# Optimization experiments

Measured on AMD Instinct MI355X. Metric: run time of the kernel, lower is better.

The kernel has to match this reference:

```python
import jax, jax.numpy as jnp
import numpy as np

NEG_SLOPE = 0.1

def mlp(x, w1, b1, w2, b2):
    # MLP(sizes): Linear -> LeakyReLU(0.1) -> Linear
    return jax.nn.leaky_relu(x @ w1 + b1, NEG_SLOPE) @ w2 + b2

def _seg_mean(vals, idx, n):
    s = jax.ops.segment_sum(vals, idx, num_segments=n)
    cnt = jax.ops.segment_sum(jnp.ones((vals.shape[0],), vals.dtype), idx, num_segments=n)
    return s / jnp.maximum(cnt, 1.0)[:, None]

def setup_inputs() -> dict:
    key = jax.random.key(0)
    ks = iter(jax.random.split(key, 40))
    N, F, H, E = 100000, 64, 128, 800000
    Ha = H // 2  # hidden_dim/2 = 64
    def lin(k, i, o):
        k1, k2 = jax.random.split(k)
        return (jax.random.normal(k1, (i, o), jnp.float32) * (1.0 / np.sqrt(i)),
                jax.random.normal(k2, (o,), jnp.float32) * 0.01)
    inp = {}
    inp['feat'] = jax.random.normal(next(ks), (N, F), jnp.float32)
    inp['pi_feat'] = jax.random.normal(next(ks), (N, 4), jnp.float32)
    inp['level'] = jax.random.uniform(next(ks), (N, 1), jnp.float32)
    inp['bit_position'] = jax.random.uniform(next(ks), (E, 1), jnp.float32)
    inp['is_po'] = jax.random.randint(next(ks), (N,), 0, 2, jnp.int32)
    inp['is_module'] = jax.random.randint(next(ks), (N,), 0, 2, jnp.int32)
    inp['src_m'] = jax.random.randint(next(ks), (E,), 0, N, jnp.int32)
    inp['dst_m'] = jax.random.randint(next(ks), (E,), 0, N, jnp.int32)
    inp['src_g'] = jax.random.randint(next(ks), (E,), 0, N, jnp.int32)
    inp['dst_g'] = jax.random.randint(next(ks), (E,), 0, N, jnp.int32)
    # mlp_pi: 4 -> H/2 -> H
    inp['pi_w1'], inp['pi_b1'] = lin(next(ks), 4, Ha)
    inp['pi_w2'], inp['pi_b2'] = lin(next(ks), Ha, H)
    # mlp_neigh_module: H + F + 1 -> H/2 -> H
    inp['nm_w1'], inp['nm_b1'] = lin(next(ks), H + F + 1, Ha)
    inp['nm_w2'], inp['nm_b2'] = lin(next(ks), Ha, H)
    # mlp_neigh_gate: H + F -> H/2 -> H
    inp['ng_w1'], inp['ng_b1'] = lin(next(ks), H + F, Ha)
    inp['ng_w2'], inp['ng_b2'] = lin(next(ks), Ha, H)
    # mlp_global: 1 -> H/2 -> H
    inp['g_w1'], inp['g_b1'] = lin(next(ks), 1, Ha)
    inp['g_w2'], inp['g_b2'] = lin(next(ks), Ha, H)
    # mlp_out: 2H -> H -> 1
    inp['o_w1'], inp['o_b1'] = lin(next(ks), 2 * H, H)
    inp['o_w2'], inp['o_b2'] = lin(next(ks), H, 1)
    return inp

def reference(feat, pi_feat, level, bit_position,
              pi_w1, pi_b1, pi_w2, pi_b2,
              nm_w1, nm_b1, nm_w2, nm_b2,
              ng_w1, ng_b1, ng_w2, ng_b2,
              g_w1, g_b1, g_w2, g_b2,
              o_w1, o_b1, o_w2, o_b2,
              is_po, is_module, src_m, dst_m, src_g, dst_g):
    N = feat.shape[0]
    # PI init embedding (mlp_pi)
    h0 = mlp(pi_feat, pi_w1, pi_b1, pi_w2, pi_b2)            # [N, H]
    # module-edge message passing: m = src h, pos = bit_position; mean reduce
    m = h0[src_m]                                            # [E, H] irregular gather
    neigh_m = _seg_mean(m, dst_m, N)                         # [N, H]
    pos_m = _seg_mean(bit_position, dst_m, N)                # [N, 1]
    # nodes_func_module, agg_choice==0: cat(neigh, pos, feat) -> mlp_neigh_module
    h_m = mlp(jnp.concatenate([neigh_m, pos_m, feat], axis=1), nm_w1, nm_b1, nm_w2, nm_b2)
    # gate-edge message passing
    neigh_g = _seg_mean(h0[src_g], dst_g, N)                 # [N, H]
    h_g = mlp(jnp.concatenate([neigh_g, feat], axis=1), ng_w1, ng_b1, ng_w2, ng_b2)
    # ReLU on non-PO nodes only
    keep = (is_po != 1)[:, None]
    h_m = jnp.where(keep, jax.nn.relu(h_m), h_m)
    h_g = jnp.where(keep, jax.nn.relu(h_g), h_g)
    # per-node-type update (hetero apply_nodes)
    h = jnp.where((is_module == 1)[:, None], h_m, h_g)       # [N, H]
    # global branch + readout
    hg = mlp(level, g_w1, g_b1, g_w2, g_b2)                  # [N, H]
    out = mlp(jnp.concatenate([h, hg], axis=1), o_w1, o_b1, o_w2, o_b2)  # [N, 1]
    return out
```

## Files before the change

### kernel.cpp

```cpp
#include <hip/hip_runtime.h>

typedef __bf16 bf16x8 __attribute__((ext_vector_type(8)));
typedef float f32x4 __attribute__((ext_vector_type(4)));
typedef unsigned short u16;
typedef unsigned int u32;
typedef unsigned long long u64;

__device__ __forceinline__ u16 f2b(float f) {
  return __builtin_bit_cast(u16, (__bf16)f);
}
__device__ __forceinline__ float b2f_lo(u32 pk) {
  return __builtin_bit_cast(float, pk << 16);
}
__device__ __forceinline__ float b2f_hi(u32 pk) {
  return __builtin_bit_cast(float, pk & 0xffff0000u);
}
__device__ __forceinline__ float leaky(float x) { return x > 0.f ? x : 0.1f * x; }
__device__ __forceinline__ f32x4 mfma16(bf16x8 a, bf16x8 b, f32x4 c) {
  return __builtin_amdgcn_mfma_f32_16x16x32_bf16(a, b, c, 0, 0, 0);
}

#define P64 72
#define P128 136
#define CAP 16
#define RSTRIDE 32

#define SBLK 256
#define PBLK 256

__global__ __launch_bounds__(256) void k_zero(int* rec, int* spillcnt, int N) {
  int n = blockIdx.x * 256 + threadIdx.x;
  if (n < N) {
    rec[(size_t)n * RSTRIDE] = 0;
    rec[(size_t)n * RSTRIDE + 1] = 0;
  }
  if (n == 0) *spillcnt = 0;
}

__global__ __launch_bounds__(256) void k_prep(
    const float* nm_w1, const float* ng_w1, const float* nm_w2, const float* ng_w2,
    const float* o_w1, const float* o_b1, const float* g_w2, const float* g_b2,
    const float* pi_w2, const float* pi_b2, const int* is_module,
    u16* wt_yc, float* bias_y, u16* wt_f1m, u16* wt_f1g, float* w_pos,
    u16* wt2m, u16* wt2g, u16* wt_oh, u16* gt, float* bp, u32* mbits, int N) {
  int i = blockIdx.x * 256 + threadIdx.x;
  if (i < 9216) {
    int ty = i / 4608, rem = i % 4608, n = rem / P64, k = rem % P64;
    float v = 0.f;
    if (k < 64) {
      const float* w1 = ty ? ng_w1 : nm_w1;
      for (int t = 0; t < 128; t++) v += pi_w2[k * 128 + t] * w1[t * 64 + n];
    }
    wt_yc[i] = f2b(v);
    return;
  }
  i -= 9216;
  if (i < 128) {
    int ty = i >> 6, n = i & 63;
    const float* w1 = ty ? ng_w1 : nm_w1;
    float v = 0.f;
    for (int t = 0; t < 128; t++) v += pi_b2[t] * w1[t * 64 + n];
    bias_y[i] = v;
    return;
  }
  i -= 128;
  if (i < 4608) {
    int n = i / P64, k = i % P64;
    wt_f1m[i] = f2b(k < 64 ? nm_w1[(129 + k) * 64 + n] : 0.f);
    return;
  }
  i -= 4608;
  if (i < 4608) {
    int n = i / P64, k = i % P64;
    wt_f1g[i] = f2b(k < 64 ? ng_w1[(128 + k) * 64 + n] : 0.f);
    return;
  }
  i -= 4608;
  if (i < 64) { w_pos[i] = nm_w1[128 * 64 + i]; return; }
  i -= 64;
  if (i < 9216) {
    int n = i / P64, k = i % P64;
    wt2m[i] = f2b(k < 64 ? nm_w2[k * 128 + n] : 0.f);
    return;
  }
  i -= 9216;
  if (i < 9216) {
    int n = i / P64, k = i % P64;
    wt2g[i] = f2b(k < 64 ? ng_w2[k * 128 + n] : 0.f);
    return;
  }
  i -= 9216;
  if (i < 17408) {
    int n = i / P128, k = i % P128;
    wt_oh[i] = f2b(k < 128 ? o_w1[k * 128 + n] : 0.f);
    return;
  }
  i -= 17408;
  if (i < 9216) {
    int n = i / P64, k = i % P64;
    float v = 0.f;
    if (k < 64)
      for (int t = 0; t < 128; t++) v += g_w2[k * 128 + t] * o_w1[(128 + t) * 128 + n];
    gt[i] = f2b(v);
    return;
  }
  i -= 9216;
  if (i < 128) {
    float s = o_b1[i];
    for (int t = 0; t < 128; t++) s += g_b2[t] * o_w1[(128 + t) * 128 + i];
    bp[i] = s;
    return;
  }
  i -= 128;
  {
    int n = i;
    int lane = threadIdx.x & 63;
    bool v = (n < N) && (is_module[n] == 1);
    u64 b = __ballot(v);
    if (lane == 0 && n < N) mbits[n >> 5] = (u32)b;
    if (lane == 32 && n < N) mbits[n >> 5] = (u32)(b >> 32);
  }
}

__global__ __launch_bounds__(512) void k_mid(
    const int* src_m, const int* dst_m, const int* src_g, const int* dst_g,
    const u32* mbits, const float* bitpos, int* rec, u64* spill, int* spillcnt,
    int E,
    const float* pf, const float* feat, const float* pi_w1, const float* pi_b1,
    const u16* wt_yc_g, const float* bias_y, const u16* wt_f1m_g, const u16* wt_f1g_g,
    const float* nm_b1, const float* ng_b1, u16* y0, u16* f1, int N) {
  __shared__ __align__(16) u16 wyc[2][64 * P64];
  __shared__ __align__(16) u16 wf[2][64 * P64];
  __shared__ __align__(16) u16 tbuf[8][16 * P64];

  if (blockIdx.x < SBLK) {
    int tid = blockIdx.x * 512 + threadIdx.x;
    const int STR = SBLK * 512;
    for (int v0 = tid; v0 < E; v0 += STR * 4) {
      int dd[8], ss[8];
      float bb[8];
      bool el[8];
#pragma unroll
      for (int k = 0; k < 4; k++) {
        int vt = v0 + k * STR;
        bool vv = vt < E;
#pragma unroll
        for (int j = 0; j < 2; j++) {
          int x = k * 2 + j;
          el[x] = false;
          dd[x] = 0; ss[x] = 0; bb[x] = 0.f;
          if (vv) {
            int e = vt * 2 + j;
            int d = (e < E) ? dst_m[e] : dst_g[e - E];
            dd[x] = d;
            bool bit = (mbits[d >> 5] >> (d & 31)) & 1;
            el[x] = (e < E) ? bit : !bit;
            if (el[x]) {
              if (e < E) { ss[x] = src_m[e]; bb[x] = bitpos[e]; }
              else ss[x] = src_g[e - E];
            }
          }
        }
      }
      int cc[8];
#pragma unroll
      for (int x = 0; x < 8; x++)
        if (el[x]) cc[x] = atomicAdd(&rec[(size_t)dd[x] * RSTRIDE], 1);
#pragma unroll
      for (int x = 0; x < 8; x++) {
        if (!el[x]) continue;
        int vt = v0 + (x >> 1) * STR;
        int e = vt * 2 + (x & 1);
        int d = dd[x], s = ss[x], c = cc[x];
        if (e < E) {
          if (c < CAP) {
            int bp12 = (int)(bb[x] * 4096.f);
            if (bp12 > 4095) bp12 = 4095;
            rec[(size_t)d * RSTRIDE + 2 + c] = (s << 12) | bp12;
          } else {
            int p = atomicAdd(spillcnt, 1);
            spill[p] = ((u64)(u32)d << 32) | (u32)s;
            atomicAdd((float*)&rec[(size_t)d * RSTRIDE + 1], bb[x]);
          }
        } else {
          if (c < CAP) {
            rec[(size_t)d * RSTRIDE + 2 + c] = s << 12;
          } else {
            int p = atomicAdd(spillcnt, 1);
            spill[p] = ((u64)(u32)d << 32) | (u32)s;
          }
        }
      }
    }
    return;
  }

  int pb = blockIdx.x - SBLK;
  for (int i = threadIdx.x; i < 2304; i += 512) {
    ((u32*)wyc[0])[i] = ((const u32*)wt_yc_g)[i];
    ((u32*)wyc[1])[i] = ((const u32*)wt_yc_g)[2304 + i];
    ((u32*)wf[0])[i] = ((const u32*)wt_f1m_g)[i];
    ((u32*)wf[1])[i] = ((const u32*)wt_f1g_g)[i];
  }

  int lane = threadIdx.x & 63, wv = threadIdx.x >> 6;
  int lid = lane & 15, q = lane >> 4;

  bf16x8 w1f[4];
#pragma unroll
  for (int nt = 0; nt < 4; nt++) {
    bf16x8 f;
#pragma unroll
    for (int j = 0; j < 8; j++) {
      int k = q * 8 + j;
      f[j] = (__bf16)((k < 4) ? pi_w1[k * 64 + nt * 16 + lid] : 0.f);
    }
    w1f[nt] = f;
  }
  __syncthreads();

  int nbat = (N + 15) >> 4;
  for (int b0 = pb * 8; b0 < nbat; b0 += PBLK * 8) {
    int b = b0 + wv;
    int batch = b < nbat ? b : nbat - 1;
    int id = batch * 16 + lid;
    if (id >= N) id = N - 1;

    bf16x8 a;
#pragma unroll
    for (int j = 0; j < 8; j++)
      a[j] = (__bf16)((q == 0 && j < 4) ? pf[(size_t)id * 4 + j] : 0.f);
    f32x4 z1[4];
#pragma unroll
    for (int nt = 0; nt < 4; nt++) {
      f32x4 c = {0.f, 0.f, 0.f, 0.f};
      z1[nt] = mfma16(a, w1f[nt], c);
    }
    __syncthreads();
#pragma unroll
    for (int nt = 0; nt < 4; nt++) {
      float bb = pi_b1[nt * 16 + lid];
#pragma unroll
      for (int r = 0; r < 4; r++)
        tbuf[wv][(q * 4 + r) * P64 + nt * 16 + lid] = f2b(leaky(z1[nt][r] + bb));
    }
    __syncthreads();
    bf16x8 a20 = *(const bf16x8*)&tbuf[wv][lid * P64 + q * 8];
    bf16x8 a21 = *(const bf16x8*)&tbuf[wv][lid * P64 + 32 + q * 8];

    int idr_[4];
#pragma unroll
    for (int r = 0; r < 4; r++) {
      int ii = batch * 16 + q * 4 + r;
      idr_[r] = ii < N ? ii : N - 1;
    }

#pragma unroll
    for (int ty = 0; ty < 2; ty++) {
#pragma unroll
      for (int nt = 0; nt < 4; nt++) {
        f32x4 c = {0.f, 0.f, 0.f, 0.f};
        c = mfma16(a20, *(const bf16x8*)&wyc[ty][(nt * 16 + lid) * P64 + q * 8], c);
        c = mfma16(a21, *(const bf16x8*)&wyc[ty][(nt * 16 + lid) * P64 + 32 + q * 8], c);
        float by = bias_y[ty * 64 + nt * 16 + lid];
#pragma unroll
        for (int r = 0; r < 4; r++)
          y0[(size_t)idr_[r] * 128 + ty * 64 + nt * 16 + lid] = f2b(c[r] + by);
      }
    }

    bf16x8 af[2];
#pragma unroll
    for (int kt = 0; kt < 2; kt++) {
      const float4* p = (const float4*)(feat + (size_t)id * 64 + kt * 32 + q * 8);
      float4 xa = p[0], xb = p[1];
      bf16x8 f;
      f[0] = (__bf16)xa.x; f[1] = (__bf16)xa.y; f[2] = (__bf16)xa.z; f[3] = (__bf16)xa.w;
      f[4] = (__bf16)xb.x; f[5] = (__bf16)xb.y; f[6] = (__bf16)xb.z; f[7] = (__bf16)xb.w;
      af[kt] = f;
    }
#pragma unroll
    for (int nt = 0; nt < 4; nt++) {
      f32x4 cm = {0.f, 0.f, 0.f, 0.f}, cg = {0.f, 0.f, 0.f, 0.f};
#pragma unroll
      for (int kt = 0; kt < 2; kt++) {
        cm = mfma16(af[kt], *(const bf16x8*)&wf[0][(nt * 16 + lid) * P64 + kt * 32 + q * 8], cm);
        cg = mfma16(af[kt], *(const bf16x8*)&wf[1][(nt * 16 + lid) * P64 + kt * 32 + q * 8], cg);
      }
      float bm = nm_b1[nt * 16 + lid], bg = ng_b1[nt * 16 + lid];
#pragma unroll
      for (int r = 0; r < 4; r++) {
        int idr = idr_[r];
        bool mod = (mbits[idr >> 5] >> (idr & 31)) & 1;
        f1[(size_t)idr * 64 + nt * 16 + lid] = f2b(mod ? cm[r] + bm : cg[r] + bg);
      }
    }
  }
}

__global__ __launch_bounds__(256) void k_gather(const u16* y0, const int* rec,
                                                const u64* spill, const int* spillcnt,
                                                const u32* mbits, const u16* f1,
                                                const float* w_pos, u16* z1a, int N) {
  int n = (blockIdx.x * 256 + threadIdx.x) >> 6;
  int lane = threadIdx.x & 63;
  if (n >= N) return;
  bool mod = (mbits[n >> 5] >> (n & 31)) & 1;
  int g = lane >> 4, l16 = lane & 15;
  int rv = (lane < 18) ? rec[(size_t)n * RSTRIDE + lane] : 0;
  int cnt = __shfl(rv, 0);
  float pspill = __builtin_bit_cast(float, __shfl(rv, 1));
  int inl = cnt < CAP ? cnt : CAP;
  float myb = 0.f;
  if (mod && lane >= 2 && lane < 18 && (lane - 2) < inl)
    myb = (float)(rv & 4095) * (1.f / 4096.f);
  const u32* yrow = (const u32*)y0;
  int halfo = mod ? 0 : 32;
  float a00 = 0.f, a01 = 0.f, a10 = 0.f, a11 = 0.f;
  for (int j = 0; j < inl; j += 4) {
    int e = j + g;
    if (e < inl) {
      int s = (int)(((u32)__shfl(rv, 2 + e)) >> 12);
      u64 pk = *(const u64*)(yrow + (size_t)s * 64 + halfo + 2 * l16);
      u32 p0 = (u32)pk, p1 = (u32)(pk >> 32);
      a00 += b2f_lo(p0); a01 += b2f_hi(p0);
      a10 += b2f_lo(p1); a11 += b2f_hi(p1);
    }
  }
  if (cnt > CAP) {
    int sc = *spillcnt;
    int idx = 0;
    for (int base = 0; base < sc; base += 64) {
      int i = base + lane;
      u64 ent = (i < sc) ? spill[i] : 0xffffffffffffffffull;
      bool m = ((int)(ent >> 32) == n);
      u64 bal = __ballot(m);
      int slo = (int)(ent & 0xffffffffu);
      while (bal) {
        int l = __ffsll((long long)bal) - 1;
        bal &= bal - 1;
        int s = __shfl(slo, l);
        if ((idx & 3) == g) {
          u64 pk = *(const u64*)(yrow + (size_t)s * 64 + halfo + 2 * l16);
          u32 p0 = (u32)pk, p1 = (u32)(pk >> 32);
          a00 += b2f_lo(p0); a01 += b2f_hi(p0);
          a10 += b2f_lo(p1); a11 += b2f_hi(p1);
        }
        idx++;
      }
    }
  }
  a00 += __shfl_xor(a00, 16); a00 += __shfl_xor(a00, 32);
  a01 += __shfl_xor(a01, 16); a01 += __shfl_xor(a01, 32);
  a10 += __shfl_xor(a10, 16); a10 += __shfl_xor(a10, 32);
  a11 += __shfl_xor(a11, 16); a11 += __shfl_xor(a11, 32);
#pragma unroll
  for (int off = 1; off < 64; off <<= 1) myb += __shfl_xor(myb, off);
  float psum = pspill + myb;
  float inv = 1.f / (float)(cnt > 1 ? cnt : 1);
  if (lane < 16) {
    u64 fp2 = *(const u64*)(((const u32*)f1) + (size_t)n * 32 + 2 * l16);
    u32 f0 = (u32)fp2, f1v = (u32)(fp2 >> 32);
    float z00 = a00 * inv + b2f_lo(f0);
    float z01 = a01 * inv + b2f_hi(f0);
    float z10 = a10 * inv + b2f_lo(f1v);
    float z11 = a11 * inv + b2f_hi(f1v);
    if (mod) {
      float pm = psum * inv;
      float4 wp = ((const float4*)w_pos)[l16];
      z00 += pm * wp.x; z01 += pm * wp.y;
      z10 += pm * wp.z; z11 += pm * wp.w;
    }
    u32 r0 = (u32)f2b(leaky(z00)) | ((u32)f2b(leaky(z01)) << 16);
    u32 r1 = (u32)f2b(leaky(z10)) | ((u32)f2b(leaky(z11)) << 16);
    *(u64*)(((u32*)z1a) + (size_t)n * 32 + 2 * l16) = ((u64)r1 << 32) | r0;
  }
}

__global__ __launch_bounds__(512) void k_tail(const u16* z1a, const u16* wt2m_g,
                                              const u16* wt2g_g, const float* nm_b2,
                                              const float* ng_b2, const u32* mbits,
                                              const int* is_po, const float* level,
                                              const float* g_w1, const float* g_b1,
                                              const u16* wt_oh_g, const u16* gt_g,
                                              const float* bp_g, const float* o_w2,
                                              const float* o_b2, float* out, int N) {
  __shared__ __align__(16) u16 w2[2][128 * P64];
  __shared__ __align__(16) u16 wt_oh[128 * P128];
  __shared__ __align__(16) u16 gt[128 * P64];
  __shared__ __align__(16) u16 tbuf[8][16 * P128];
  for (int i = threadIdx.x; i < 128 * P64 / 2; i += 512) {
    ((u32*)w2[0])[i] = ((const u32*)wt2m_g)[i];
    ((u32*)w2[1])[i] = ((const u32*)wt2g_g)[i];
    ((u32*)gt)[i] = ((const u32*)gt_g)[i];
  }
  for (int i = threadIdx.x; i < 128 * P128 / 2; i += 512)
    ((u32*)wt_oh)[i] = ((const u32*)wt_oh_g)[i];

  int lane = threadIdx.x & 63, wv = threadIdx.x >> 6;
  int lid = lane & 15, q = lane >> 4;
  int nbat = (N + 15) >> 4;

  float gw[2][8], gb[2][8];
#pragma unroll
  for (int kt = 0; kt < 2; kt++)
#pragma unroll
    for (int j = 0; j < 8; j++) {
      int k = kt * 32 + q * 8 + j;
      gw[kt][j] = g_w1[k];
      gb[kt][j] = g_b1[k];
    }
  float w2o[8], bpv[8];
#pragma unroll
  for (int nt = 0; nt < 8; nt++) {
    w2o[nt] = o_w2[nt * 16 + lid];
    bpv[nt] = bp_g[nt * 16 + lid];
  }
  float b2m[8], b2g[8];
#pragma unroll
  for (int nt = 0; nt < 8; nt++) {
    b2m[nt] = nm_b2[nt * 16 + lid];
    b2g[nt] = ng_b2[nt * 16 + lid];
  }
  float ob2 = o_b2[0];
  __syncthreads();

  for (int b0 = blockIdx.x * 8; b0 < nbat; b0 += gridDim.x * 8) {
    int b = b0 + wv;
    int batch = b < nbat ? b : nbat - 1;
    int id = batch * 16 + lid;
    if (id >= N) id = N - 1;

    bf16x8 a0 = *(const bf16x8*)(z1a + (size_t)id * 64 + q * 8);
    bf16x8 a1 = *(const bf16x8*)(z1a + (size_t)id * 64 + 32 + q * 8);
    bool mod_[4], kp_[4];
#pragma unroll
    for (int r = 0; r < 4; r++) {
      int ii = batch * 16 + q * 4 + r;
      if (ii >= N) ii = N - 1;
      mod_[r] = (mbits[ii >> 5] >> (ii & 31)) & 1;
      kp_[r] = (is_po[ii] != 1);
    }
    __syncthreads();
#pragma unroll
    for (int nt = 0; nt < 8; nt++) {
      f32x4 cm = {0.f, 0.f, 0.f, 0.f}, cg = {0.f, 0.f, 0.f, 0.f};
      cm = mfma16(a0, *(const bf16x8*)&w2[0][(nt * 16 + lid) * P64 + q * 8], cm);
      cm = mfma16(a1, *(const bf16x8*)&w2[0][(nt * 16 + lid) * P64 + 32 + q * 8], cm);
      cg = mfma16(a0, *(const bf16x8*)&w2[1][(nt * 16 + lid) * P64 + q * 8], cg);
      cg = mfma16(a1, *(const bf16x8*)&w2[1][(nt * 16 + lid) * P64 + 32 + q * 8], cg);
#pragma unroll
      for (int r = 0; r < 4; r++) {
        float v = mod_[r] ? cm[r] + b2m[nt] : cg[r] + b2g[nt];
        if (kp_[r]) v = fmaxf(v, 0.f);
        tbuf[wv][(q * 4 + r) * P128 + nt * 16 + lid] = f2b(v);
      }
    }
    __syncthreads();

    bf16x8 ah[4];
#pragma unroll
    for (int kt = 0; kt < 4; kt++)
      ah[kt] = *(const bf16x8*)&tbuf[wv][lid * P128 + kt * 32 + q * 8];
    float lv = level[id];
    bf16x8 ag[2];
#pragma unroll
    for (int kt = 0; kt < 2; kt++)
#pragma unroll
      for (int j = 0; j < 8; j++)
        ag[kt][j] = (__bf16)leaky(lv * gw[kt][j] + gb[kt][j]);

    f32x4 accv[8];
#pragma unroll
    for (int nt = 0; nt < 8; nt++) {
      f32x4 c = {0.f, 0.f, 0.f, 0.f};
#pragma unroll
      for (int kt = 0; kt < 4; kt++)
        c = mfma16(ah[kt], *(const bf16x8*)&wt_oh[(nt * 16 + lid) * P128 + kt * 32 + q * 8], c);
#pragma unroll
      for (int kt = 0; kt < 2; kt++)
        c = mfma16(ag[kt], *(const bf16x8*)&gt[(nt * 16 + lid) * P64 + kt * 32 + q * 8], c);
      accv[nt] = c;
    }
    float p[4];
#pragma unroll
    for (int r = 0; r < 4; r++) {
      float s = 0.f;
#pragma unroll
      for (int nt = 0; nt < 8; nt++) s += leaky(accv[nt][r] + bpv[nt]) * w2o[nt];
      p[r] = s;
    }
#pragma unroll
    for (int r = 0; r < 4; r++)
#pragma unroll
      for (int off = 1; off < 16; off <<= 1) p[r] += __shfl_xor(p[r], off, 16);
    if (lid == 0) {
#pragma unroll
      for (int r = 0; r < 4; r++) {
        int idr = batch * 16 + q * 4 + r;
        if (idr >= N) idr = N - 1;
        out[idr] = p[r] + ob2;
      }
    }
  }
}

extern "C" void kernel_launch(void* const* d_in, const int* in_sizes, int n_in,
                              void* d_out, int out_size, void* d_ws, size_t ws_size,
                              hipStream_t stream) {
  const float* feat = (const float*)d_in[0];
  const float* pi_feat = (const float*)d_in[1];
  const float* level = (const float*)d_in[2];
  const float* bitpos = (const float*)d_in[3];
  const int* is_po = (const int*)d_in[4];
  const int* is_module = (const int*)d_in[5];
  const int* src_m = (const int*)d_in[6];
  const int* dst_m = (const int*)d_in[7];
  const int* src_g = (const int*)d_in[8];
  const int* dst_g = (const int*)d_in[9];
  const float* pi_w1 = (const float*)d_in[10];
  const float* pi_b1 = (const float*)d_in[11];
  const float* pi_w2 = (const float*)d_in[12];
  const float* pi_b2 = (const float*)d_in[13];
  const float* nm_w1 = (const float*)d_in[14];
  const float* nm_b1 = (const float*)d_in[15];
  const float* nm_w2 = (const float*)d_in[16];
  const float* nm_b2 = (const float*)d_in[17];
  const float* ng_w1 = (const float*)d_in[18];
  const float* ng_b1 = (const float*)d_in[19];
  const float* ng_w2 = (const float*)d_in[20];
  const float* ng_b2 = (const float*)d_in[21];
  const float* g_w1 = (const float*)d_in[22];
  const float* g_b1 = (const float*)d_in[23];
  const float* g_w2 = (const float*)d_in[24];
  const float* g_b2 = (const float*)d_in[25];
  const float* o_w1 = (const float*)d_in[26];
  const float* o_b1 = (const float*)d_in[27];
  const float* o_w2 = (const float*)d_in[28];
  const float* o_b2 = (const float*)d_in[29];

  int N = in_sizes[0] / 64;
  int E = in_sizes[3];

  char* ws = (char*)d_ws;
  size_t off = 0;
  auto alloc = [&](size_t bytes) {
    char* p = ws + off;
    off += (bytes + 255) & ~(size_t)255;
    return p;
  };
  int* rec = (int*)alloc(((size_t)N * RSTRIDE + 64) * 4);
  int* spillcnt = (int*)alloc(16);
  u64* spill = (u64*)alloc((size_t)2 * E * 8);
  u32* mbits = (u32*)alloc((size_t)((N + 31) / 32) * 4);
  u16* y0 = (u16*)alloc((size_t)N * 128 * 2);
  u16* f1 = (u16*)alloc((size_t)N * 64 * 2);
  u16* z1a = (u16*)alloc((size_t)N * 64 * 2);
  u16* wt_yc = (u16*)alloc(9216 * 2);
  float* bias_y = (float*)alloc(128 * 4);
  u16* wt_f1m = (u16*)alloc(4608 * 2);
  u16* wt_f1g = (u16*)alloc(4608 * 2);
  float* w_pos = (float*)alloc(64 * 4);
  u16* wt2m = (u16*)alloc(9216 * 2);
  u16* wt2g = (u16*)alloc(9216 * 2);
  u16* wt_oh = (u16*)alloc(17408 * 2);
  u16* gt = (u16*)alloc(9216 * 2);
  float* bp = (float*)alloc(128 * 4);

  k_zero<<<(N + 255) / 256, 256, 0, stream>>>(rec, spillcnt, N);

  int prep_items = 63808 + ((N + 63) & ~63);
  k_prep<<<(prep_items + 255) / 256, 256, 0, stream>>>(
      nm_w1, ng_w1, nm_w2, ng_w2, o_w1, o_b1, g_w2, g_b2, pi_w2, pi_b2, is_module,
      wt_yc, bias_y, wt_f1m, wt_f1g, w_pos, wt2m, wt2g, wt_oh, gt, bp, mbits, N);

  k_mid<<<SBLK + PBLK, 512, 0, stream>>>(
      src_m, dst_m, src_g, dst_g, mbits, bitpos, rec, spill, spillcnt, E,
      pi_feat, feat, pi_w1, pi_b1, wt_yc, bias_y, wt_f1m, wt_f1g,
      nm_b1, ng_b1, y0, f1, N);

  k_gather<<<(N * 64 + 255) / 256, 256, 0, stream>>>(
      y0, rec, spill, spillcnt, mbits, f1, w_pos, z1a, N);

  k_tail<<<256, 512, 0, stream>>>(z1a, wt2m, wt2g, nm_b2, ng_b2, mbits, is_po,
                                  level, g_w1, g_b1, wt_oh, gt, bp, o_w2, o_b2,
                                  (float*)d_out, N);
}
```

Before: 267.2 us.

## Fold weight prep into zero and mid kernels to drop a launch

Removes the separate k_prep launch. The is_module bitmask build moves into the zero kernel, tail-weight prep runs on 32 extra blocks of k_mid, and each node-processing block now builds the fused pi/w1 weights and biases directly in shared memory. This saves one kernel launch and its global round trip. The cost is that every one of 256 node blocks repeats a 128-term dot product per weight element, which lengthens those blocks' prologue.

```diff
diff --git a/kernel.cpp b/kernel.cpp
--- a/kernel.cpp
+++ b/kernel.cpp
@@ -25,101 +25,24 @@
 #define CAP 16
 #define RSTRIDE 32
 
+#define PREPB 32
 #define SBLK 256
 #define PBLK 256
 
-__global__ __launch_bounds__(256) void k_zero(int* rec, int* spillcnt, int N) {
+__global__ __launch_bounds__(256) void k_zero2(int* rec, int* spillcnt,
+                                               const int* is_module, u32* mbits,
+                                               int N) {
   int n = blockIdx.x * 256 + threadIdx.x;
+  int lane = threadIdx.x & 63;
+  bool v = (n < N) && (is_module[n] == 1);
+  u64 b = __ballot(v);
   if (n < N) {
     rec[(size_t)n * RSTRIDE] = 0;
     rec[(size_t)n * RSTRIDE + 1] = 0;
+    if (lane == 0) mbits[n >> 5] = (u32)b;
+    if (lane == 32) mbits[n >> 5] = (u32)(b >> 32);
   }
   if (n == 0) *spillcnt = 0;
-}
-
-__global__ __launch_bounds__(256) void k_prep(
-    const float* nm_w1, const float* ng_w1, const float* nm_w2, const float* ng_w2,
-    const float* o_w1, const float* o_b1, const float* g_w2, const float* g_b2,
-    const float* pi_w2, const float* pi_b2, const int* is_module,
-    u16* wt_yc, float* bias_y, u16* wt_f1m, u16* wt_f1g, float* w_pos,
-    u16* wt2m, u16* wt2g, u16* wt_oh, u16* gt, float* bp, u32* mbits, int N) {
-  int i = blockIdx.x * 256 + threadIdx.x;
-  if (i < 9216) {
-    int ty = i / 4608, rem = i % 4608, n = rem / P64, k = rem % P64;
-    float v = 0.f;
-    if (k < 64) {
-      const float* w1 = ty ? ng_w1 : nm_w1;
-      for (int t = 0; t < 128; t++) v += pi_w2[k * 128 + t] * w1[t * 64 + n];
-    }
-    wt_yc[i] = f2b(v);
-    return;
-  }
-  i -= 9216;
-  if (i < 128) {
-    int ty = i >> 6, n = i & 63;
-    const float* w1 = ty ? ng_w1 : nm_w1;
-    float v = 0.f;
-    for (int t = 0; t < 128; t++) v += pi_b2[t] * w1[t * 64 + n];
-    bias_y[i] = v;
-    return;
-  }
-  i -= 128;
-  if (i < 4608) {
-    int n = i / P64, k = i % P64;
-    wt_f1m[i] = f2b(k < 64 ? nm_w1[(129 + k) * 64 + n] : 0.f);
-    return;
-  }
-  i -= 4608;
-  if (i < 4608) {
-    int n = i / P64, k = i % P64;
-    wt_f1g[i] = f2b(k < 64 ? ng_w1[(128 + k) * 64 + n] : 0.f);
-    return;
-  }
-  i -= 4608;
-  if (i < 64) { w_pos[i] = nm_w1[128 * 64 + i]; return; }
-  i -= 64;
-  if (i < 9216) {
-    int n = i / P64, k = i % P64;
-    wt2m[i] = f2b(k < 64 ? nm_w2[k * 128 + n] : 0.f);
-    return;
-  }
-  i -= 9216;
-  if (i < 9216) {
-    int n = i / P64, k = i % P64;
-    wt2g[i] = f2b(k < 64 ? ng_w2[k * 128 + n] : 0.f);
-    return;
-  }
-  i -= 9216;
-  if (i < 17408) {
-    int n = i / P128, k = i % P128;
-    wt_oh[i] = f2b(k < 128 ? o_w1[k * 128 + n] : 0.f);
-    return;
-  }
-  i -= 17408;
-  if (i < 9216) {
-    int n = i / P64, k = i % P64;
-    float v = 0.f;
-    if (k < 64)
-      for (int t = 0; t < 128; t++) v += g_w2[k * 128 + t] * o_w1[(128 + t) * 128 + n];
-    gt[i] = f2b(v);
-    return;
-  }
-  i -= 9216;
-  if (i < 128) {
-    float s = o_b1[i];
-    for (int t = 0; t < 128; t++) s += g_b2[t] * o_w1[(128 + t) * 128 + i];
-    bp[i] = s;
-    return;
-  }
-  i -= 128;
-  {
-    int n = i;
-    int lane = threadIdx.x & 63;
-    bool v = (n < N) && (is_module[n] == 1);
-    u64 b = __ballot(v);
-    if (lane == 0 && n < N) mbits[n >> 5] = (u32)b;
-    if (lane == 32 && n < N) mbits[n >> 5] = (u32)(b >> 32);
-  }
 }
 
 __global__ __launch_bounds__(512) void k_mid(
@@ -127,14 +50,62 @@
     const u32* mbits, const float* bitpos, int* rec, u64* spill, int* spillcnt,
     int E,
     const float* pf, const float* feat, const float* pi_w1, const float* pi_b1,
-    const u16* wt_yc_g, const float* bias_y, const u16* wt_f1m_g, const u16* wt_f1g_g,
-    const float* nm_b1, const float* ng_b1, u16* y0, u16* f1, int N) {
+    const float* pi_w2, const float* pi_b2,
+    const float* nm_w1, const float* ng_w1, const float* nm_b1, const float* ng_b1,
+    const float* nm_w2, const float* ng_w2, const float* o_w1, const float* o_b1,
+    const float* g_w2, const float* g_b2,
+    u16* y0, u16* f1,
+    u16* wt2m, u16* wt2g, u16* wt_oh, u16* gt, float* bp, float* w_pos, int N) {
   __shared__ __align__(16) u16 wyc[2][64 * P64];
   __shared__ __align__(16) u16 wf[2][64 * P64];
   __shared__ __align__(16) u16 tbuf[8][16 * P64];
-
-  if (blockIdx.x < SBLK) {
-    int tid = blockIdx.x * 512 + threadIdx.x;
+  __shared__ float bias_l[128];
+
+  if (blockIdx.x < PREPB) {
+    const int TOTAL = 9216 + 9216 + 17408 + 9216 + 128 + 64;
+    for (int it = blockIdx.x * 512 + threadIdx.x; it < TOTAL; it += PREPB * 512) {
+      int i = it;
+      if (i < 9216) {
+        int n = i / P64, k = i % P64;
+        wt2m[i] = f2b(k < 64 ? nm_w2[k * 128 + n] : 0.f);
+        continue;
+      }
+      i -= 9216;
+      if (i < 9216) {
+        int n = i / P64, k = i % P64;
+        wt2g[i] = f2b(k < 64 ? ng_w2[k * 128 + n] : 0.f);
+        continue;
+      }
+      i -= 9216;
+      if (i < 17408) {
+        int n = i / P128, k = i % P128;
+        wt_oh[i] = f2b(k < 128 ? o_w1[k * 128 + n] : 0.f);
+        continue;
+      }
+      i -= 17408;
+      if (i < 9216) {
+        int n = i / P64, k = i % P64;
+        float v = 0.f;
+        if (k < 64)
+          for (int t = 0; t < 128; t++) v += g_w2[k * 128 + t] * o_w1[(128 + t) * 128 + n];
+        gt[i] = f2b(v);
+        continue;
+      }
+      i -= 9216;
+      if (i < 128) {
+        float s = o_b1[i];
+        for (int t = 0; t < 128; t++) s += g_b2[t] * o_w1[(128 + t) * 128 + i];
+        bp[i] = s;
+        continue;
+      }
+      i -= 128;
+      w_pos[i] = nm_w1[128 * 64 + i];
+    }
+    return;
+  }
+
+  if (blockIdx.x < PREPB + SBLK) {
+    int tid = (blockIdx.x - PREPB) * 512 + threadIdx.x;
     const int STR = SBLK * 512;
     for (int v0 = tid; v0 < E; v0 += STR * 4) {
       int dd[8], ss[8];
@@ -195,12 +166,27 @@
     return;
   }
 
-  int pb = blockIdx.x - SBLK;
-  for (int i = threadIdx.x; i < 2304; i += 512) {
-    ((u32*)wyc[0])[i] = ((const u32*)wt_yc_g)[i];
-    ((u32*)wyc[1])[i] = ((const u32*)wt_yc_g)[2304 + i];
-    ((u32*)wf[0])[i] = ((const u32*)wt_f1m_g)[i];
-    ((u32*)wf[1])[i] = ((const u32*)wt_f1g_g)[i];
+  int pb = blockIdx.x - PREPB - SBLK;
+  for (int i = threadIdx.x; i < 4608; i += 512) {
+    int n = i / P64, k = i % P64;
+    wf[0][i] = f2b(k < 64 ? nm_w1[(129 + k) * 64 + n] : 0.f);
+    wf[1][i] = f2b(k < 64 ? ng_w1[(128 + k) * 64 + n] : 0.f);
+  }
+  for (int i = threadIdx.x; i < 9216; i += 512) {
+    int ty = i / 4608, rem = i % 4608, n = rem / P64, k = rem % P64;
+    float v = 0.f;
+    if (k < 64) {
+      const float* w1 = ty ? ng_w1 : nm_w1;
+      for (int t = 0; t < 128; t++) v += pi_w2[k * 128 + t] * w1[t * 64 + n];
+    }
+    wyc[ty][rem] = f2b(v);
+  }
+  for (int i = threadIdx.x; i < 128; i += 512) {
+    int ty = i >> 6, n = i & 63;
+    const float* w1 = ty ? ng_w1 : nm_w1;
+    float v = 0.f;
+    for (int t = 0; t < 128; t++) v += pi_b2[t] * w1[t * 64 + n];
+    bias_l[i] = v;
   }
 
   int lane = threadIdx.x & 63, wv = threadIdx.x >> 6;
@@ -262,7 +248,7 @@
         f32x4 c = {0.f, 0.f, 0.f, 0.f};
         c = mfma16(a20, *(const bf16x8*)&wyc[ty][(nt * 16 + lid) * P64 + q * 8], c);
         c = mfma16(a21, *(const bf16x8*)&wyc[ty][(nt * 16 + lid) * P64 + 32 + q * 8], c);
-        float by = bias_y[ty * 64 + nt * 16 + lid];
+        float by = bias_l[ty * 64 + nt * 16 + lid];
 #pragma unroll
         for (int r = 0; r < 4; r++)
           y0[(size_t)idr_[r] * 128 + ty * 64 + nt * 16 + lid] = f2b(c[r] + by);
@@ -556,10 +542,6 @@
   u16* y0 = (u16*)alloc((size_t)N * 128 * 2);
   u16* f1 = (u16*)alloc((size_t)N * 64 * 2);
   u16* z1a = (u16*)alloc((size_t)N * 64 * 2);
-  u16* wt_yc = (u16*)alloc(9216 * 2);
-  float* bias_y = (float*)alloc(128 * 4);
-  u16* wt_f1m = (u16*)alloc(4608 * 2);
-  u16* wt_f1g = (u16*)alloc(4608 * 2);
   float* w_pos = (float*)alloc(64 * 4);
   u16* wt2m = (u16*)alloc(9216 * 2);
   u16* wt2g = (u16*)alloc(9216 * 2);
@@ -567,17 +549,14 @@
   u16* gt = (u16*)alloc(9216 * 2);
   float* bp = (float*)alloc(128 * 4);
 
-  k_zero<<<(N + 255) / 256, 256, 0, stream>>>(rec, spillcnt, N);
-
-  int prep_items = 63808 + ((N + 63) & ~63);
-  k_prep<<<(prep_items + 255) / 256, 256, 0, stream>>>(
-      nm_w1, ng_w1, nm_w2, ng_w2, o_w1, o_b1, g_w2, g_b2, pi_w2, pi_b2, is_module,
-      wt_yc, bias_y, wt_f1m, wt_f1g, w_pos, wt2m, wt2g, wt_oh, gt, bp, mbits, N);
-
-  k_mid<<<SBLK + PBLK, 512, 0, stream>>>(
+  k_zero2<<<(N + 255) / 256, 256, 0, stream>>>(rec, spillcnt, is_module, mbits, N);
+
+  k_mid<<<PREPB + SBLK + PBLK, 512, 0, stream>>>(
       src_m, dst_m, src_g, dst_g, mbits, bitpos, rec, spill, spillcnt, E,
-      pi_feat, feat, pi_w1, pi_b1, wt_yc, bias_y, wt_f1m, wt_f1g,
-      nm_b1, ng_b1, y0, f1, N);
+      pi_feat, feat, pi_w1, pi_b1, pi_w2, pi_b2,
+      nm_w1, ng_w1, nm_b1, ng_b1,
+      nm_w2, ng_w2, o_w1, o_b1, g_w2, g_b2,
+      y0, f1, wt2m, wt2g, wt_oh, gt, bp, w_pos, N);
 
   k_gather<<<(N * 64 + 255) / 256, 256, 0, stream>>>(
       y0, rec, spill, spillcnt, mbits, f1, w_pos, z1a, N);
```

New measurement: 405.0 us. 51.6% more time.
